# Kernel tuning notes

Measured on AMD Instinct MI355X. Metric: run time of the kernel, lower is better.

Reference implementation:

```python
import jax, jax.numpy as jnp
import numpy as np

B, QDIM, KDIM, EMBED, HEADS = 8, 256, 256, 512, 8
HIMG, WIMG = 32, 32
HEAD_DIM = EMBED // HEADS


def setup_inputs() -> dict:
    key = jax.random.key(0)
    ks = jax.random.split(key, 8)
    scale_q = 1.0 / np.sqrt(QDIM)
    scale_k = 1.0 / np.sqrt(KDIM)
    return {
        "query": jax.random.normal(ks[0], (B, QDIM, HIMG, WIMG), jnp.float32),
        "key": jax.random.normal(ks[1], (B, KDIM, HIMG, WIMG), jnp.float32),
        "Wq": jax.random.uniform(ks[2], (EMBED, QDIM), jnp.float32, -scale_q, scale_q),
        "bq": jax.random.uniform(ks[3], (EMBED,), jnp.float32, -scale_q, scale_q),
        "Wk": jax.random.uniform(ks[4], (EMBED, KDIM), jnp.float32, -scale_k, scale_k),
        "bk": jax.random.uniform(ks[5], (EMBED,), jnp.float32, -scale_k, scale_k),
        "Wv": jax.random.uniform(ks[6], (EMBED, KDIM), jnp.float32, -scale_k, scale_k),
        "bv": jax.random.uniform(ks[7], (EMBED,), jnp.float32, -scale_k, scale_k),
    }


def reference(query, key, Wq, bq, Wk, bk, Wv, bv):
    b, _, h, w = query.shape
    s = h * w
    # (B, C, H, W) -> (B, S, C)
    q = query.transpose(0, 2, 3, 1).reshape(b, s, QDIM)
    kv = key.transpose(0, 2, 3, 1).reshape(b, s, KDIM)
    q = q @ Wq.T + bq            # (B, S, E)
    k = kv @ Wk.T + bk
    v = kv @ Wv.T + bv
    # split heads: (B, S, H, D) -> (B, H, S, D)
    q = q.reshape(b, s, HEADS, HEAD_DIM).transpose(0, 2, 1, 3)
    k = k.reshape(b, s, HEADS, HEAD_DIM).transpose(0, 2, 1, 3)
    v = v.reshape(b, s, HEADS, HEAD_DIM).transpose(0, 2, 1, 3)
    scores = jnp.einsum("bhqd,bhkd->bhqk", q, k) / np.sqrt(HEAD_DIM)
    # causal additive mask: -inf above the diagonal
    causal = jnp.tril(jnp.ones((s, s), dtype=bool))
    scores = jnp.where(causal, scores, -jnp.inf)
    attn = jax.nn.softmax(scores, axis=-1)
    x = jnp.einsum("bhqk,bhkd->bhqd", attn, v)   # (B, H, S, D)
    # (B, H, S, D) -> (B, H, D, S) -> (B, E, H_img, W_img)
    out = x.transpose(0, 1, 3, 2).reshape(b, EMBED, h, w)
    return out
```

## Files before the change

kernel.cpp:

```cpp
#include <hip/hip_runtime.h>
#include <hip/hip_bf16.h>

#define BATCH 8
#define CDIM 256
#define SEQ 1024
#define EMB 512
#define NHEAD 8
#define HDIM 64

typedef __bf16 bf16x8 __attribute__((ext_vector_type(8)));
typedef float f32x4 __attribute__((ext_vector_type(4)));
typedef float f32x16 __attribute__((ext_vector_type(16)));

static __device__ __forceinline__ unsigned short f2b(float f) {
    __hip_bfloat16 h = __float2bfloat16(f);
    return __builtin_bit_cast(unsigned short, h);
}

static __device__ __forceinline__ f32x4 mfma16(bf16x8 a, bf16x8 b, f32x4 c) {
    return __builtin_amdgcn_mfma_f32_16x16x32_bf16(a, b, c, 0, 0, 0);
}
static __device__ __forceinline__ f32x16 mfma32(bf16x8 a, bf16x8 b, f32x16 c) {
    return __builtin_amdgcn_mfma_f32_32x32x16_bf16(a, b, c, 0, 0, 0);
}

__global__ __launch_bounds__(256) void prep_w(
    const float* __restrict__ Wq, const float* __restrict__ Wk,
    const float* __restrict__ Wv, unsigned short* __restrict__ Wc)
{
    int pz = blockIdx.z;
    const float* W = (pz == 0) ? Wq : (pz == 1 ? Wk : Wv);
    int idx = (blockIdx.x * 256 + threadIdx.x) * 8;
    float4 v0 = *(const float4*)&W[idx];
    float4 v1 = *(const float4*)&W[idx + 4];
    int4 pk;
    pk.x = (int)((unsigned)f2b(v0.x) | ((unsigned)f2b(v0.y) << 16));
    pk.y = (int)((unsigned)f2b(v0.z) | ((unsigned)f2b(v0.w) << 16));
    pk.z = (int)((unsigned)f2b(v1.x) | ((unsigned)f2b(v1.y) << 16));
    pk.w = (int)((unsigned)f2b(v1.z) | ((unsigned)f2b(v1.w) << 16));
    *(int4*)&Wc[(size_t)pz * (EMB * CDIM) + idx] = pk;
}

__global__ __launch_bounds__(256) void transpose_cvt(
    const float* __restrict__ query, const float* __restrict__ key_,
    unsigned short* __restrict__ Xq, unsigned short* __restrict__ Xk)
{
    __shared__ alignas(16) unsigned short sT[64 * 66];
    int tid = threadIdx.x;
    int s0 = blockIdx.x * 64, c0 = blockIdx.y * 64;
    int z = blockIdx.z;
    int which = z >> 3, b = z & 7;
    const float* src = which ? key_ : query;
    unsigned short* dst = which ? Xk : Xq;

#pragma unroll
    for (int p = 0; p < 4; ++p) {
        int c = (tid >> 4) + p * 16;
        int sch = tid & 15;
        float4 v = *(const float4*)&src[((size_t)b * CDIM + c0 + c) * SEQ + s0 + sch * 4];
        sT[c * 66 + sch * 4 + 0] = f2b(v.x);
        sT[c * 66 + sch * 4 + 1] = f2b(v.y);
        sT[c * 66 + sch * 4 + 2] = f2b(v.z);
        sT[c * 66 + sch * 4 + 3] = f2b(v.w);
    }
    __syncthreads();
#pragma unroll
    for (int p = 0; p < 4; ++p) {
        int s = (tid >> 4) + p * 16;
        int cch = tid & 15;
        unsigned short e0 = sT[(cch * 4 + 0) * 66 + s];
        unsigned short e1 = sT[(cch * 4 + 1) * 66 + s];
        unsigned short e2 = sT[(cch * 4 + 2) * 66 + s];
        unsigned short e3 = sT[(cch * 4 + 3) * 66 + s];
        uint2 pk;
        pk.x = (unsigned)e0 | ((unsigned)e1 << 16);
        pk.y = (unsigned)e2 | ((unsigned)e3 << 16);
        *(uint2*)&dst[((size_t)b * SEQ + s0 + s) * CDIM + c0 + cch * 4] = pk;
    }
}

__global__ __launch_bounds__(256) void proj_kernel(
    const unsigned short* __restrict__ Xq, const unsigned short* __restrict__ Xk,
    const unsigned short* __restrict__ Wc,
    const float* __restrict__ bq, const float* __restrict__ bk,
    const float* __restrict__ bv,
    unsigned short* __restrict__ Qb, unsigned short* __restrict__ Kb,
    unsigned short* __restrict__ Vt)
{
    __shared__ alignas(16) unsigned short sX[128 * 72];
    __shared__ alignas(16) unsigned short sW[128 * 72];
    int tid = threadIdx.x;
    int n0 = blockIdx.x * 128;
    int m0 = blockIdx.y * 128;
    int proj = n0 >> 9;
    const unsigned short* X = (proj == 0) ? Xq : Xk;
    const float* bias = (proj == 0) ? bq : (proj == 1 ? bk : bv);

    int lane = tid & 63, w = tid >> 6;
    int l16 = lane & 15, lhi = lane >> 4;
    int wr = w >> 1, wc = w & 1;

    f32x4 zero = {0.f, 0.f, 0.f, 0.f};
    f32x4 acc[4][4];
#pragma unroll
    for (int i = 0; i < 4; ++i)
#pragma unroll
        for (int j = 0; j < 4; ++j) acc[i][j] = zero;

    for (int kt = 0; kt < 4; ++kt) {
        int c0 = kt * 64;
        if (kt) __syncthreads();
#pragma unroll
        for (int p = 0; p < 4; ++p) {
            int row = (tid >> 3) + p * 32, ch = tid & 7;
            *(int4*)&sX[row * 72 + ch * 8] =
                *(const int4*)&X[(size_t)(m0 + row) * CDIM + c0 + ch * 8];
            *(int4*)&sW[row * 72 + ch * 8] =
                *(const int4*)&Wc[(size_t)(n0 + row) * CDIM + c0 + ch * 8];
        }
        __syncthreads();
        const unsigned short* tA = (proj == 2) ? &sX[0] : &sW[0];
        const unsigned short* tB = (proj == 2) ? &sW[0] : &sX[0];
#pragma unroll
        for (int kk = 0; kk < 2; ++kk) {
            bf16x8 af[4], bfr[4];
#pragma unroll
            for (int i = 0; i < 4; ++i)
                af[i] = *(const bf16x8*)&tA[(wr * 64 + i * 16 + l16) * 72 + kk * 32 + lhi * 8];
#pragma unroll
            for (int j = 0; j < 4; ++j)
                bfr[j] = *(const bf16x8*)&tB[(wc * 64 + j * 16 + l16) * 72 + kk * 32 + lhi * 8];
#pragma unroll
            for (int i = 0; i < 4; ++i)
#pragma unroll
                for (int j = 0; j < 4; ++j)
                    acc[i][j] = mfma16(af[i], bfr[j], acc[i][j]);
        }
    }

    if (proj != 2) {
        unsigned short* dst = proj ? Kb : Qb;
        float scale = proj ? 1.0f : (0.125f * 1.44269504f);
#pragma unroll
        for (int i = 0; i < 4; ++i) {
            int e0 = (n0 & 511) + wr * 64 + i * 16 + lhi * 4;
            float4 bv4 = *(const float4*)&bias[e0];
            int hh = e0 >> 6, dd = e0 & 63;
#pragma unroll
            for (int j = 0; j < 4; ++j) {
                int mg = m0 + wc * 64 + j * 16 + l16;
                int bb = mg >> 10, s = mg & 1023;
                uint2 pk;
                pk.x = (unsigned)f2b((acc[i][j][0] + bv4.x) * scale) |
                       ((unsigned)f2b((acc[i][j][1] + bv4.y) * scale) << 16);
                pk.y = (unsigned)f2b((acc[i][j][2] + bv4.z) * scale) |
                       ((unsigned)f2b((acc[i][j][3] + bv4.w) * scale) << 16);
                *(uint2*)&dst[(((size_t)bb * NHEAD + hh) * SEQ + s) * HDIM + dd] = pk;
            }
        }
    } else {
#pragma unroll
        for (int j = 0; j < 4; ++j) {
            int e = (n0 & 511) + wc * 64 + j * 16 + l16;
            float bval = bias[e];
            int hh = e >> 6, dd = e & 63;
#pragma unroll
            for (int i = 0; i < 4; ++i) {
                int mg = m0 + wr * 64 + i * 16 + lhi * 4;
                int bb = mg >> 10, s = mg & 1023;
                uint2 pk;
                pk.x = (unsigned)f2b(acc[i][j][0] + bval) |
                       ((unsigned)f2b(acc[i][j][1] + bval) << 16);
                pk.y = (unsigned)f2b(acc[i][j][2] + bval) |
                       ((unsigned)f2b(acc[i][j][3] + bval) << 16);
                *(uint2*)&Vt[(((size_t)bb * NHEAD + hh) * HDIM + dd) * SEQ + s] = pk;
            }
        }
    }
}

__global__ __launch_bounds__(64, 2) void attn_kernel(
    const unsigned short* __restrict__ Qb, const unsigned short* __restrict__ Kb,
    const unsigned short* __restrict__ Vt, float* __restrict__ out)
{
    int lane = threadIdx.x;
    int l32 = lane & 31, hi = lane >> 5;
    int bh = blockIdx.x;
    int qt = (int)(gridDim.y - 1 - blockIdx.y);
    int b = bh >> 3, h = bh & 7;
    int q0 = qt * 32;

    const unsigned short* Qhead = Qb + (size_t)bh * SEQ * HDIM;
    const unsigned short* Khead = Kb + (size_t)bh * SEQ * HDIM;
    const unsigned short* Vhead = Vt + (size_t)bh * HDIM * SEQ;

    bf16x8 qf[4];
#pragma unroll
    for (int dblk = 0; dblk < 4; ++dblk)
        qf[dblk] = *(const bf16x8*)&Qhead[(size_t)(q0 + l32) * HDIM + dblk * 16 + hi * 8];

    f32x16 o0, o1;
#pragma unroll
    for (int r = 0; r < 16; ++r) { o0[r] = 0.f; o1[r] = 0.f; }
    float m = -1e30f, l = 0.f;

    auto loadKV = [&](int kt, bf16x8 (&ka)[4], bf16x8 (&va)[2][2]) {
        int k0 = kt * 32;
#pragma unroll
        for (int dblk = 0; dblk < 4; ++dblk)
            ka[dblk] = *(const bf16x8*)&Khead[(size_t)(k0 + l32) * HDIM + dblk * 16 + hi * 8];
#pragma unroll
        for (int t = 0; t < 2; ++t)
#pragma unroll
            for (int ks = 0; ks < 2; ++ks)
                va[t][ks] = *(const bf16x8*)
                    &Vhead[(size_t)(t * 32 + l32) * SEQ + k0 + ks * 16 + hi * 8];
    };

    auto compute = [&](int kt, const bf16x8 (&ka)[4], const bf16x8 (&va)[2][2]) {
        f32x16 st;
#pragma unroll
        for (int r = 0; r < 16; ++r) st[r] = 0.f;
#pragma unroll
        for (int dblk = 0; dblk < 4; ++dblk)
            st = mfma32(ka[dblk], qf[dblk], st);

        if (kt == qt) {
#pragma unroll
            for (int r = 0; r < 16; ++r) {
                int kk = (r & 3) + 8 * (r >> 2) + 4 * hi;
                if (kk > l32) st[r] = -1e38f;
            }
        }

        float t8[8];
#pragma unroll
        for (int r = 0; r < 8; ++r) t8[r] = fmaxf(st[r], st[r + 8]);
        float t4[4];
#pragma unroll
        for (int r = 0; r < 4; ++r) t4[r] = fmaxf(t8[r], t8[r + 4]);
        float t2a = fmaxf(t4[0], t4[2]), t2b = fmaxf(t4[1], t4[3]);
        float tmax = fmaxf(t2a, t2b);
        tmax = fmaxf(tmax, __shfl_xor(tmax, 32));
        if (!__all(tmax <= m + 8.0f)) {
            float mnew = fmaxf(m, tmax);
            float corr = __builtin_amdgcn_exp2f(m - mnew);
#pragma unroll
            for (int r = 0; r < 16; ++r) { o0[r] *= corr; o1[r] *= corr; }
            l *= corr;
            m = mnew;
        }
        float p[16];
#pragma unroll
        for (int r = 0; r < 16; ++r) p[r] = __builtin_amdgcn_exp2f(st[r] - m);
        float s8[8];
#pragma unroll
        for (int r = 0; r < 8; ++r) s8[r] = p[r] + p[r + 8];
        float s4[4];
#pragma unroll
        for (int r = 0; r < 4; ++r) s4[r] = s8[r] + s8[r + 4];
        float ts = (s4[0] + s4[2]) + (s4[1] + s4[3]);
        ts += __shfl_xor(ts, 32);
        l += ts;

        unsigned u[8];
#pragma unroll
        for (int i = 0; i < 8; ++i) {
            unsigned r_;
            asm("v_cvt_pk_bf16_f32 %0, %1, %2" : "=v"(r_) : "v"(p[2 * i]), "v"(p[2 * i + 1]));
            u[i] = r_;
        }
        asm("v_permlane32_swap_b32 %0, %1" : "+v"(u[0]), "+v"(u[2]));
        asm("v_permlane32_swap_b32 %0, %1" : "+v"(u[1]), "+v"(u[3]));
        asm("v_permlane32_swap_b32 %0, %1" : "+v"(u[4]), "+v"(u[6]));
        asm("v_permlane32_swap_b32 %0, %1" : "+v"(u[5]), "+v"(u[7]));
        uint4 pw0 = {u[0], u[1], u[2], u[3]};
        uint4 pw1 = {u[4], u[5], u[6], u[7]};
        bf16x8 pb0 = __builtin_bit_cast(bf16x8, pw0);
        bf16x8 pb1 = __builtin_bit_cast(bf16x8, pw1);

        o0 = mfma32(va[0][0], pb0, o0);
        o1 = mfma32(va[1][0], pb0, o1);
        o0 = mfma32(va[0][1], pb1, o0);
        o1 = mfma32(va[1][1], pb1, o1);
    };

    int nt = qt + 1;
    bf16x8 kaA[4], vaA[2][2], kaB[4], vaB[2][2];
    loadKV(0, kaA, vaA);
    int kt = 0;
    while (true) {
        if (kt + 1 < nt) loadKV(kt + 1, kaB, vaB);
        compute(kt, kaA, vaA);
        if (++kt >= nt) break;
        if (kt + 1 < nt) loadKV(kt + 1, kaA, vaA);
        compute(kt, kaB, vaB);
        if (++kt >= nt) break;
    }

    float inv = 1.0f / l;
    size_t base = ((size_t)b * EMB + h * HDIM) * SEQ + q0 + l32;
#pragma unroll
    for (int r = 0; r < 16; ++r) {
        int d0 = (r & 3) + 8 * (r >> 2) + 4 * hi;
        out[base + (size_t)d0 * SEQ] = o0[r] * inv;
        out[base + (size_t)(d0 + 32) * SEQ] = o1[r] * inv;
    }
}

extern "C" void kernel_launch(void* const* d_in, const int* in_sizes, int n_in,
                              void* d_out, int out_size, void* d_ws, size_t ws_size,
                              hipStream_t stream) {
    const float* query = (const float*)d_in[0];
    const float* key_  = (const float*)d_in[1];
    const float* Wq    = (const float*)d_in[2];
    const float* bq    = (const float*)d_in[3];
    const float* Wk    = (const float*)d_in[4];
    const float* bk    = (const float*)d_in[5];
    const float* Wv    = (const float*)d_in[6];
    const float* bv    = (const float*)d_in[7];
    float* out = (float*)d_out;

    char* ws = (char*)d_ws;
    unsigned short* Qb = (unsigned short*)(ws);
    unsigned short* Kb = (unsigned short*)(ws + 8388608);
    unsigned short* Vt = (unsigned short*)(ws + 16777216);
    unsigned short* Xq = (unsigned short*)(ws + 25165824);
    unsigned short* Xk = (unsigned short*)(ws + 29360128);
    unsigned short* Wc = (unsigned short*)((char*)d_out + 16777216 - 1048576);

    prep_w<<<dim3(64, 1, 3), 256, 0, stream>>>(Wq, Wk, Wv, Wc);
    transpose_cvt<<<dim3(SEQ / 64, CDIM / 64, 2 * BATCH), 256, 0, stream>>>(query, key_, Xq, Xk);
    proj_kernel<<<dim3(12, 64), 256, 0, stream>>>(Xq, Xk, Wc, bq, bk, bv, Qb, Kb, Vt);
    attn_kernel<<<dim3(BATCH * NHEAD, SEQ / 32), 64, 0, stream>>>(Qb, Kb, Vt, out);
}
```

Before: 140.9 us.

## Merge prep kernels, swizzle LDS with direct loads, and process 64-key attention tiles

Three independent changes land together. The weight conversion and input transpose are merged into one launch, and their outputs are stored with an XOR swizzle. The projection GEMM then fills LDS through global_load_lds direct loads into unpadded swizzled tiles, which drops the register round-trip and the padding. The attention loop now handles 64 keys per step, with a 32-key tail for the diagonal, and raises MFMA priority with s_setprio. This halves softmax reductions and rescale checks per key, at the cost of more registers for the larger K/V prefetch buffers.

```diff
diff --git a/kernel.cpp b/kernel.cpp
--- a/kernel.cpp
+++ b/kernel.cpp
@@ -24,31 +24,40 @@
     return __builtin_amdgcn_mfma_f32_32x32x16_bf16(a, b, c, 0, 0, 0);
 }
 
-__global__ __launch_bounds__(256) void prep_w(
+static __device__ __forceinline__ void gload16(const void* g, void* l) {
+    __builtin_amdgcn_global_load_lds(
+        (const __attribute__((address_space(1))) unsigned int*)g,
+        (__attribute__((address_space(3))) unsigned int*)l, 16, 0, 0);
+}
+
+__global__ __launch_bounds__(256) void prep_kernel(
+    const float* __restrict__ query, const float* __restrict__ key_,
     const float* __restrict__ Wq, const float* __restrict__ Wk,
-    const float* __restrict__ Wv, unsigned short* __restrict__ Wc)
+    const float* __restrict__ Wv,
+    unsigned short* __restrict__ Xq, unsigned short* __restrict__ Xk,
+    unsigned short* __restrict__ Wc)
 {
-    int pz = blockIdx.z;
-    const float* W = (pz == 0) ? Wq : (pz == 1 ? Wk : Wv);
-    int idx = (blockIdx.x * 256 + threadIdx.x) * 8;
-    float4 v0 = *(const float4*)&W[idx];
-    float4 v1 = *(const float4*)&W[idx + 4];
-    int4 pk;
-    pk.x = (int)((unsigned)f2b(v0.x) | ((unsigned)f2b(v0.y) << 16));
-    pk.y = (int)((unsigned)f2b(v0.z) | ((unsigned)f2b(v0.w) << 16));
-    pk.z = (int)((unsigned)f2b(v1.x) | ((unsigned)f2b(v1.y) << 16));
-    pk.w = (int)((unsigned)f2b(v1.z) | ((unsigned)f2b(v1.w) << 16));
-    *(int4*)&Wc[(size_t)pz * (EMB * CDIM) + idx] = pk;
-}
-
-__global__ __launch_bounds__(256) void transpose_cvt(
-    const float* __restrict__ query, const float* __restrict__ key_,
-    unsigned short* __restrict__ Xq, unsigned short* __restrict__ Xk)
-{
+    int tid = threadIdx.x;
+    int z = blockIdx.z;
+    if (z >= 16) {
+        int pz = z - 16;
+        const float* W = (pz == 0) ? Wq : (pz == 1 ? Wk : Wv);
+        int lin = blockIdx.y * 16 + blockIdx.x;
+        int idx = (lin * 256 + tid) * 8;
+        int e7 = (idx >> 8) & 7;
+        float4 v0 = *(const float4*)&W[idx];
+        float4 v1 = *(const float4*)&W[idx + 4];
+        int4 pk;
+        pk.x = (int)((unsigned)f2b(v0.x) | ((unsigned)f2b(v0.y) << 16));
+        pk.y = (int)((unsigned)f2b(v0.z) | ((unsigned)f2b(v0.w) << 16));
+        pk.z = (int)((unsigned)f2b(v1.x) | ((unsigned)f2b(v1.y) << 16));
+        pk.w = (int)((unsigned)f2b(v1.z) | ((unsigned)f2b(v1.w) << 16));
+        int dsti = (idx & ~255) | ((idx & 255) ^ (e7 << 3));
+        *(int4*)&Wc[(size_t)pz * (EMB * CDIM) + dsti] = pk;
+        return;
+    }
     __shared__ alignas(16) unsigned short sT[64 * 66];
-    int tid = threadIdx.x;
     int s0 = blockIdx.x * 64, c0 = blockIdx.y * 64;
-    int z = blockIdx.z;
     int which = z >> 3, b = z & 7;
     const float* src = which ? key_ : query;
     unsigned short* dst = which ? Xk : Xq;
@@ -75,7 +84,8 @@
         uint2 pk;
         pk.x = (unsigned)e0 | ((unsigned)e1 << 16);
         pk.y = (unsigned)e2 | ((unsigned)e3 << 16);
-        *(uint2*)&dst[((size_t)b * SEQ + s0 + s) * CDIM + c0 + cch * 4] = pk;
+        int col = (cch * 4) ^ ((s & 7) << 3);
+        *(uint2*)&dst[((size_t)b * SEQ + s0 + s) * CDIM + c0 + col] = pk;
     }
 }
 
@@ -87,8 +97,8 @@
     unsigned short* __restrict__ Qb, unsigned short* __restrict__ Kb,
     unsigned short* __restrict__ Vt)
 {
-    __shared__ alignas(16) unsigned short sX[128 * 72];
-    __shared__ alignas(16) unsigned short sW[128 * 72];
+    __shared__ alignas(16) unsigned short sX[128 * 64];
+    __shared__ alignas(16) unsigned short sW[128 * 64];
     int tid = threadIdx.x;
     int n0 = blockIdx.x * 128;
     int m0 = blockIdx.y * 128;
@@ -99,6 +109,7 @@
     int lane = tid & 63, w = tid >> 6;
     int l16 = lane & 15, lhi = lane >> 4;
     int wr = w >> 1, wc = w & 1;
+    int lrow = lane >> 3, lcb = (lane & 7) * 8;
 
     f32x4 zero = {0.f, 0.f, 0.f, 0.f};
     f32x4 acc[4][4];
@@ -111,12 +122,11 @@
         int c0 = kt * 64;
         if (kt) __syncthreads();
 #pragma unroll
-        for (int p = 0; p < 4; ++p) {
-            int row = (tid >> 3) + p * 32, ch = tid & 7;
-            *(int4*)&sX[row * 72 + ch * 8] =
-                *(const int4*)&X[(size_t)(m0 + row) * CDIM + c0 + ch * 8];
-            *(int4*)&sW[row * 72 + ch * 8] =
-                *(const int4*)&Wc[(size_t)(n0 + row) * CDIM + c0 + ch * 8];
+        for (int i = 0; i < 4; ++i) {
+            int seg = i * 4 + w;
+            int row = seg * 8 + lrow;
+            gload16(&X[(size_t)(m0 + row) * CDIM + c0 + lcb], &sX[seg * 512]);
+            gload16(&Wc[(size_t)(n0 + row) * CDIM + c0 + lcb], &sW[seg * 512]);
         }
         __syncthreads();
         const unsigned short* tA = (proj == 2) ? &sX[0] : &sW[0];
@@ -125,11 +135,15 @@
         for (int kk = 0; kk < 2; ++kk) {
             bf16x8 af[4], bfr[4];
 #pragma unroll
-            for (int i = 0; i < 4; ++i)
-                af[i] = *(const bf16x8*)&tA[(wr * 64 + i * 16 + l16) * 72 + kk * 32 + lhi * 8];
-#pragma unroll
-            for (int j = 0; j < 4; ++j)
-                bfr[j] = *(const bf16x8*)&tB[(wc * 64 + j * 16 + l16) * 72 + kk * 32 + lhi * 8];
+            for (int i = 0; i < 4; ++i) {
+                int r = wr * 64 + i * 16 + l16;
+                af[i] = *(const bf16x8*)&tA[r * 64 + ((kk * 32 + lhi * 8) ^ ((r & 7) << 3))];
+            }
+#pragma unroll
+            for (int j = 0; j < 4; ++j) {
+                int r = wc * 64 + j * 16 + l16;
+                bfr[j] = *(const bf16x8*)&tB[r * 64 + ((kk * 32 + lhi * 8) ^ ((r & 7) << 3))];
+            }
 #pragma unroll
             for (int i = 0; i < 4; ++i)
 #pragma unroll
@@ -204,43 +218,82 @@
     for (int r = 0; r < 16; ++r) { o0[r] = 0.f; o1[r] = 0.f; }
     float m = -1e30f, l = 0.f;
 
-    auto loadKV = [&](int kt, bf16x8 (&ka)[4], bf16x8 (&va)[2][2]) {
-        int k0 = kt * 32;
+    bf16x8 kA[8], kB[8], vv[8], vtl[4];
+
+    auto loadK64 = [&](int k0, bf16x8 (&ka)[8]) {
+#pragma unroll
+        for (int h2 = 0; h2 < 2; ++h2)
+#pragma unroll
+            for (int dblk = 0; dblk < 4; ++dblk)
+                ka[h2 * 4 + dblk] = *(const bf16x8*)
+                    &Khead[(size_t)(k0 + h2 * 32 + l32) * HDIM + dblk * 16 + hi * 8];
+    };
+    auto loadK32 = [&](int k0, bf16x8 (&ka)[8]) {
 #pragma unroll
         for (int dblk = 0; dblk < 4; ++dblk)
             ka[dblk] = *(const bf16x8*)&Khead[(size_t)(k0 + l32) * HDIM + dblk * 16 + hi * 8];
-#pragma unroll
-        for (int t = 0; t < 2; ++t)
+    };
+    auto loadV64 = [&](int k0) {
+#pragma unroll
+        for (int t2 = 0; t2 < 2; ++t2)
+#pragma unroll
+            for (int ks = 0; ks < 4; ++ks)
+                vv[t2 * 4 + ks] = *(const bf16x8*)
+                    &Vhead[(size_t)(t2 * 32 + l32) * SEQ + k0 + ks * 16 + hi * 8];
+    };
+    auto loadV32 = [&](int k0) {
+#pragma unroll
+        for (int t2 = 0; t2 < 2; ++t2)
 #pragma unroll
             for (int ks = 0; ks < 2; ++ks)
-                va[t][ks] = *(const bf16x8*)
-                    &Vhead[(size_t)(t * 32 + l32) * SEQ + k0 + ks * 16 + hi * 8];
-    };
-
-    auto compute = [&](int kt, const bf16x8 (&ka)[4], const bf16x8 (&va)[2][2]) {
-        f32x16 st;
-#pragma unroll
-        for (int r = 0; r < 16; ++r) st[r] = 0.f;
-#pragma unroll
-        for (int dblk = 0; dblk < 4; ++dblk)
-            st = mfma32(ka[dblk], qf[dblk], st);
-
-        if (kt == qt) {
+                vtl[t2 * 2 + ks] = *(const bf16x8*)
+                    &Vhead[(size_t)(t2 * 32 + l32) * SEQ + k0 + ks * 16 + hi * 8];
+    };
+    auto packP = [&](const f32x16& st, bf16x8& pbA, bf16x8& pbB) {
+        unsigned u[8];
+#pragma unroll
+        for (int i = 0; i < 8; ++i) {
+            unsigned r_;
+            asm("v_cvt_pk_bf16_f32 %0, %1, %2" : "=v"(r_) : "v"(st[2 * i]), "v"(st[2 * i + 1]));
+            u[i] = r_;
+        }
+        asm("v_permlane32_swap_b32 %0, %1" : "+v"(u[0]), "+v"(u[2]));
+        asm("v_permlane32_swap_b32 %0, %1" : "+v"(u[1]), "+v"(u[3]));
+        asm("v_permlane32_swap_b32 %0, %1" : "+v"(u[4]), "+v"(u[6]));
+        asm("v_permlane32_swap_b32 %0, %1" : "+v"(u[5]), "+v"(u[7]));
+        uint4 w0 = {u[0], u[1], u[2], u[3]};
+        uint4 w1 = {u[4], u[5], u[6], u[7]};
+        pbA = __builtin_bit_cast(bf16x8, w0);
+        pbB = __builtin_bit_cast(bf16x8, w1);
+    };
+
+    auto tile64 = [&](const bf16x8 (&ka)[8], bool maskDiag) {
+        f32x16 st0, st1;
+#pragma unroll
+        for (int r = 0; r < 16; ++r) { st0[r] = 0.f; st1[r] = 0.f; }
+        __builtin_amdgcn_s_setprio(1);
+#pragma unroll
+        for (int dblk = 0; dblk < 4; ++dblk) st0 = mfma32(ka[dblk], qf[dblk], st0);
+#pragma unroll
+        for (int dblk = 0; dblk < 4; ++dblk) st1 = mfma32(ka[4 + dblk], qf[dblk], st1);
+        __builtin_amdgcn_s_setprio(0);
+        if (maskDiag) {
 #pragma unroll
             for (int r = 0; r < 16; ++r) {
-                int kk = (r & 3) + 8 * (r >> 2) + 4 * hi;
-                if (kk > l32) st[r] = -1e38f;
+                int cd = (r & 3) + 8 * (r >> 2) + 4 * hi;
+                if (cd > l32) st1[r] = -1e38f;
             }
         }
-
+        float t16[16];
+#pragma unroll
+        for (int r = 0; r < 16; ++r) t16[r] = fmaxf(st0[r], st1[r]);
         float t8[8];
 #pragma unroll
-        for (int r = 0; r < 8; ++r) t8[r] = fmaxf(st[r], st[r + 8]);
+        for (int r = 0; r < 8; ++r) t8[r] = fmaxf(t16[r], t16[r + 8]);
         float t4[4];
 #pragma unroll
         for (int r = 0; r < 4; ++r) t4[r] = fmaxf(t8[r], t8[r + 4]);
-        float t2a = fmaxf(t4[0], t4[2]), t2b = fmaxf(t4[1], t4[3]);
-        float tmax = fmaxf(t2a, t2b);
+        float tmax = fmaxf(fmaxf(t4[0], t4[2]), fmaxf(t4[1], t4[3]));
         tmax = fmaxf(tmax, __shfl_xor(tmax, 32));
         if (!__all(tmax <= m + 8.0f)) {
             float mnew = fmaxf(m, tmax);
@@ -250,52 +303,104 @@
             l *= corr;
             m = mnew;
         }
-        float p[16];
-#pragma unroll
-        for (int r = 0; r < 16; ++r) p[r] = __builtin_amdgcn_exp2f(st[r] - m);
+#pragma unroll
+        for (int r = 0; r < 16; ++r) {
+            st0[r] = __builtin_amdgcn_exp2f(st0[r] - m);
+            st1[r] = __builtin_amdgcn_exp2f(st1[r] - m);
+        }
+        float s16[16];
+#pragma unroll
+        for (int r = 0; r < 16; ++r) s16[r] = st0[r] + st1[r];
         float s8[8];
 #pragma unroll
-        for (int r = 0; r < 8; ++r) s8[r] = p[r] + p[r + 8];
+        for (int r = 0; r < 8; ++r) s8[r] = s16[r] + s16[r + 8];
         float s4[4];
 #pragma unroll
         for (int r = 0; r < 4; ++r) s4[r] = s8[r] + s8[r + 4];
         float ts = (s4[0] + s4[2]) + (s4[1] + s4[3]);
         ts += __shfl_xor(ts, 32);
         l += ts;
-
-        unsigned u[8];
-#pragma unroll
-        for (int i = 0; i < 8; ++i) {
-            unsigned r_;
-            asm("v_cvt_pk_bf16_f32 %0, %1, %2" : "=v"(r_) : "v"(p[2 * i]), "v"(p[2 * i + 1]));
-            u[i] = r_;
-        }
-        asm("v_permlane32_swap_b32 %0, %1" : "+v"(u[0]), "+v"(u[2]));
-        asm("v_permlane32_swap_b32 %0, %1" : "+v"(u[1]), "+v"(u[3]));
-        asm("v_permlane32_swap_b32 %0, %1" : "+v"(u[4]), "+v"(u[6]));
-        asm("v_permlane32_swap_b32 %0, %1" : "+v"(u[5]), "+v"(u[7]));
-        uint4 pw0 = {u[0], u[1], u[2], u[3]};
-        uint4 pw1 = {u[4], u[5], u[6], u[7]};
-        bf16x8 pb0 = __builtin_bit_cast(bf16x8, pw0);
-        bf16x8 pb1 = __builtin_bit_cast(bf16x8, pw1);
-
-        o0 = mfma32(va[0][0], pb0, o0);
-        o1 = mfma32(va[1][0], pb0, o1);
-        o0 = mfma32(va[0][1], pb1, o0);
-        o1 = mfma32(va[1][1], pb1, o1);
-    };
-
-    int nt = qt + 1;
-    bf16x8 kaA[4], vaA[2][2], kaB[4], vaB[2][2];
-    loadKV(0, kaA, vaA);
-    int kt = 0;
-    while (true) {
-        if (kt + 1 < nt) loadKV(kt + 1, kaB, vaB);
-        compute(kt, kaA, vaA);
-        if (++kt >= nt) break;
-        if (kt + 1 < nt) loadKV(kt + 1, kaA, vaA);
-        compute(kt, kaB, vaB);
-        if (++kt >= nt) break;
+        bf16x8 pb0, pb1, pb2, pb3;
+        packP(st0, pb0, pb1);
+        packP(st1, pb2, pb3);
+        __builtin_amdgcn_s_setprio(1);
+        o0 = mfma32(vv[0], pb0, o0); o1 = mfma32(vv[4], pb0, o1);
+        o0 = mfma32(vv[1], pb1, o0); o1 = mfma32(vv[5], pb1, o1);
+        o0 = mfma32(vv[2], pb2, o0); o1 = mfma32(vv[6], pb2, o1);
+        o0 = mfma32(vv[3], pb3, o0); o1 = mfma32(vv[7], pb3, o1);
+        __builtin_amdgcn_s_setprio(0);
+    };
+
+    auto tile32 = [&](const bf16x8 (&ka)[8]) {
+        f32x16 st0;
+#pragma unroll
+        for (int r = 0; r < 16; ++r) st0[r] = 0.f;
+        __builtin_amdgcn_s_setprio(1);
+#pragma unroll
+        for (int dblk = 0; dblk < 4; ++dblk) st0 = mfma32(ka[dblk], qf[dblk], st0);
+        __builtin_amdgcn_s_setprio(0);
+#pragma unroll
+        for (int r = 0; r < 16; ++r) {
+            int cd = (r & 3) + 8 * (r >> 2) + 4 * hi;
+            if (cd > l32) st0[r] = -1e38f;
+        }
+        float t8[8];
+#pragma unroll
+        for (int r = 0; r < 8; ++r) t8[r] = fmaxf(st0[r], st0[r + 8]);
+        float t4[4];
+#pragma unroll
+        for (int r = 0; r < 4; ++r) t4[r] = fmaxf(t8[r], t8[r + 4]);
+        float tmax = fmaxf(fmaxf(t4[0], t4[2]), fmaxf(t4[1], t4[3]));
+        tmax = fmaxf(tmax, __shfl_xor(tmax, 32));
+        if (!__all(tmax <= m + 8.0f)) {
+            float mnew = fmaxf(m, tmax);
+            float corr = __builtin_amdgcn_exp2f(m - mnew);
+#pragma unroll
+            for (int r = 0; r < 16; ++r) { o0[r] *= corr; o1[r] *= corr; }
+            l *= corr;
+            m = mnew;
+        }
+#pragma unroll
+        for (int r = 0; r < 16; ++r) st0[r] = __builtin_amdgcn_exp2f(st0[r] - m);
+        float s8[8];
+#pragma unroll
+        for (int r = 0; r < 8; ++r) s8[r] = st0[r] + st0[r + 8];
+        float s4[4];
+#pragma unroll
+        for (int r = 0; r < 4; ++r) s4[r] = s8[r] + s8[r + 4];
+        float ts = (s4[0] + s4[2]) + (s4[1] + s4[3]);
+        ts += __shfl_xor(ts, 32);
+        l += ts;
+        bf16x8 pb0, pb1;
+        packP(st0, pb0, pb1);
+        __builtin_amdgcn_s_setprio(1);
+        o0 = mfma32(vtl[0], pb0, o0); o0 = mfma32(vtl[1], pb1, o0);
+        o1 = mfma32(vtl[2], pb0, o1); o1 = mfma32(vtl[3], pb1, o1);
+        __builtin_amdgcn_s_setprio(0);
+    };
+
+    int nt64 = (qt + 1) >> 1;
+    bool tail = ((qt & 1) == 0);
+
+    if (nt64 == 0) {
+        loadK32(0, kA);
+        loadV32(0);
+        tile32(kA);
+    } else {
+        loadK64(0, kA);
+        int t = 0;
+        while (true) {
+            loadV64(t * 64);
+            if (t + 1 < nt64) loadK64((t + 1) * 64, kB);
+            else if (tail) { loadK32(q0, kB); loadV32(q0); }
+            tile64(kA, (t == nt64 - 1) && !tail);
+            if (++t >= nt64) { if (tail) tile32(kB); break; }
+            loadV64(t * 64);
+            if (t + 1 < nt64) loadK64((t + 1) * 64, kA);
+            else if (tail) { loadK32(q0, kA); loadV32(q0); }
+            tile64(kB, (t == nt64 - 1) && !tail);
+            if (++t >= nt64) { if (tail) tile32(kA); break; }
+        }
     }
 
     float inv = 1.0f / l;
@@ -329,8 +434,7 @@
     unsigned short* Xk = (unsigned short*)(ws + 29360128);
     unsigned short* Wc = (unsigned short*)((char*)d_out + 16777216 - 1048576);
 
-    prep_w<<<dim3(64, 1, 3), 256, 0, stream>>>(Wq, Wk, Wv, Wc);
-    transpose_cvt<<<dim3(SEQ / 64, CDIM / 64, 2 * BATCH), 256, 0, stream>>>(query, key_, Xq, Xk);
+    prep_kernel<<<dim3(16, 4, 19), 256, 0, stream>>>(query, key_, Wq, Wk, Wv, Xq, Xk, Wc);
     proj_kernel<<<dim3(12, 64), 256, 0, stream>>>(Xq, Xk, Wc, bq, bk, bv, Qb, Kb, Vt);
     attn_kernel<<<dim3(BATCH * NHEAD, SEQ / 32), 64, 0, stream>>>(Qb, Kb, Vt, out);
 }
```

After: 147.0 us. 1.04x slower.
